# Kernel optimization log

Measured on AMD Instinct MI355X. Metric: run time of the kernel, lower is better.

The kernel has to match this reference:

```python
import jax, jax.numpy as jnp
import numpy as np

# Module hyperparameters (from init_kwargs)
H, E, K = 16, 8, 2          # heads, experts per head, top-k
P, PV = 64, 64              # q/k and v projection sizes
D = 1024                    # state / input / output size
B, T = 8, 512               # batch, sequence length (self-attention)
R = 2 * T - 1               # number of relative offsets


def setup_inputs() -> dict:
    key = jax.random.key(0)
    ks = jax.random.split(key, 9)
    std_in = 1.0 / np.sqrt(D)
    std_out = 1.0 / np.sqrt(H * PV)
    return {
        "x": jax.random.normal(ks[0], (B, T, D), jnp.float32),
        "pe": jax.random.normal(ks[1], (R, D), jnp.float32),
        "w_sel_o": jax.random.normal(ks[2], (H, E, D), jnp.float32) * std_in,
        "w_sel_v": jax.random.normal(ks[3], (H, E, D), jnp.float32) * std_in,
        "W_q": jax.random.normal(ks[4], (H, E, D, P), jnp.float32) * std_in,
        "W_k": jax.random.normal(ks[5], (H, E, D, P), jnp.float32) * std_in,
        "W_v": jax.random.normal(ks[6], (H, E, D, PV), jnp.float32) * std_in,
        "W_o": jax.random.normal(ks[7], (H, E, PV, D), jnp.float32) * std_out,
        "W_pos": jax.random.normal(ks[8], (H * P, D), jnp.float32) * std_in,
    }


def _gates(x, w_sel):
    # sigmoid selection per head, top-K experts kept with their gate values.
    logits = jnp.einsum('btd,hed->bthe', x, w_sel)
    g = jax.nn.sigmoid(logits)
    vals, idx = jax.lax.top_k(g, K)                      # [B,T,H,K]
    onehot = jax.nn.one_hot(idx, E, dtype=g.dtype)        # [B,T,H,K,E]
    return jnp.einsum('bthk,bthke->bthe', vals, onehot)   # sparse dense gates [B,T,H,E]


def _moe_proj(x, W, gates):
    # x [B,T,D], W [H,E,D,P], gates [B,T,H,E] -> [B,T,H,P]
    out = jnp.zeros(x.shape[:2] + (H, W.shape[-1]), x.dtype)
    for e in range(E):  # fixed small expert loop; avoids [B,T,H,E,P] intermediate
        out = out + gates[..., e, None] * jnp.einsum('btd,hdp->bthp', x, W[:, e])
    return out


def reference(x, pe, w_sel_o, w_sel_v, W_q, W_k, W_v, W_o, W_pos):
    # MoEUT selection sharing: q shares o's selection, k shares v's selection.
    g_qo = _gates(x, w_sel_o)
    g_kv = _gates(x, w_sel_v)

    q = _moe_proj(x, W_q, g_qo)   # [B,T,H,P]
    k = _moe_proj(x, W_k, g_kv)   # [B,T,H,P]
    v = _moe_proj(x, W_v, g_kv)   # [B,T,H,PV]

    scale = 1.0 / np.sqrt(P)
    k_pos = (pe @ W_pos.T).reshape(R, H, P)               # relative-position keys

    s_cont = jnp.einsum('bthp,bshp->bhts', q, k)          # content scores
    s_rel = jnp.einsum('bthp,rhp->bhtr', q, k_pos)        # scores over relative offsets
    t_idx = jnp.arange(T)
    rel = t_idx[None, :] - t_idx[:, None] + (T - 1)       # rel index for (t, s)
    s_pos = s_rel[:, :, t_idx[:, None], rel]              # Transformer-XL shift -> [B,H,T,T]

    scores = (s_cont + s_pos) * scale
    causal = t_idx[None, :] <= t_idx[:, None]
    scores = jnp.where(causal[None, None], scores, jnp.asarray(-1e9, scores.dtype))
    attn = jax.nn.softmax(scores, axis=-1)
    ctx = jnp.einsum('bhts,bshv->bthv', attn, v)          # [B,T,H,PV]

    # MoE output projection with o-selection
    out = jnp.zeros((x.shape[0], x.shape[1], W_o.shape[-1]), x.dtype)
    for e in range(E):
        out = out + jnp.einsum('bthv,hvd->btd', ctx * g_qo[..., e, None], W_o[:, e])
    return out
```

## Files before the change

### kernel.cpp

```cpp
#include <hip/hip_runtime.h>
#include <hip/hip_bf16.h>
#include <math.h>

#define H_ 16
#define E_ 8
#define D_ 1024
#define P_ 64
#define PV_ 64
#define B_ 8
#define T_ 512
#define R_ 1023
#define BT_ 4096
#define CAP_ 1024
#define PROWS_ 192
#define PTILES_ 4

typedef __attribute__((ext_vector_type(8))) unsigned short ushort8;
typedef __attribute__((ext_vector_type(4))) unsigned short ushort4v;
typedef __attribute__((ext_vector_type(8))) short short8;
typedef __attribute__((ext_vector_type(4))) float f32x4;

__device__ inline float bf2f(unsigned short u) {
  union { unsigned int i; float f; } c; c.i = ((unsigned int)u) << 16; return c.f;
}
__device__ inline unsigned short f2bf(float f) {
  __hip_bfloat16 h = __float2bfloat16(f);
  return *reinterpret_cast<unsigned short*>(&h);
}

__global__ void zero_cnt_kernel(int* __restrict__ cnt) {
  int i = threadIdx.x;
  if (i < 512) cnt[i] = 0;
}

__global__ __launch_bounds__(256) void xcvt_kernel(
    const float* __restrict__ x, unsigned short* __restrict__ xbu) {
  int i = blockIdx.x * 256 + threadIdx.x;
  float4 w = ((const float4*)x)[i];
  ushort4v o = {f2bf(w.x), f2bf(w.y), f2bf(w.z), f2bf(w.w)};
  *(ushort4v*)&xbu[(size_t)i * 4] = o;
}

__global__ __launch_bounds__(256) void wt_transpose_kernel(
    const float* __restrict__ wso, const float* __restrict__ wsv,
    float* __restrict__ wt) {
  __shared__ float tb[64][65];
  int ct = blockIdx.x, kt = blockIdx.y;
  int tid = threadIdx.x;
  int cl = tid >> 2, kseg = (tid & 3) * 16;
  int c = ct * 64 + cl;
  const float* src = (c < 128) ? (wso + (size_t)c * D_)
                               : (wsv + (size_t)(c - 128) * D_);
#pragma unroll
  for (int i = 0; i < 4; ++i) {
    float4 v4 = *(const float4*)&src[kt * 64 + kseg + i * 4];
    tb[cl][kseg + i * 4 + 0] = v4.x;
    tb[cl][kseg + i * 4 + 1] = v4.y;
    tb[cl][kseg + i * 4 + 2] = v4.z;
    tb[cl][kseg + i * 4 + 3] = v4.w;
  }
  __syncthreads();
  int kl = tid >> 2, cseg = (tid & 3) * 16;
#pragma unroll
  for (int i = 0; i < 4; ++i) {
    float4 o = {tb[cseg + i * 4 + 0][kl], tb[cseg + i * 4 + 1][kl],
                tb[cseg + i * 4 + 2][kl], tb[cseg + i * 4 + 3][kl]};
    *(float4*)&wt[(size_t)(kt * 64 + kl) * 256 + ct * 64 + cseg + i * 4] = o;
  }
}

__global__ __launch_bounds__(256) void gates_gemm(
    const float* __restrict__ x, const float* __restrict__ wt,
    float* __restrict__ part) {
  __shared__ __align__(16) float xs[32][256];
  int tid = threadIdx.x;
  int bt0 = blockIdx.x * 32;
  int ks = blockIdx.y;

  {
    const float4* xr = (const float4*)x;
#pragma unroll
    for (int p = 0; p < 8; ++p) {
      int idx = p * 256 + tid;
      int r = idx >> 6, k4 = idx & 63;
      ((float4*)xs[r])[k4] = xr[(size_t)(bt0 + r) * 256 + ks * 64 + k4];
    }
  }
  __syncthreads();

  int wave = tid >> 6, lane = tid & 63;
  const float4* wt4 = (const float4*)wt + (size_t)ks * 256 * 64 + lane;
  float4 acc[8];
#pragma unroll
  for (int r = 0; r < 8; ++r) acc[r] = (float4){0.f, 0.f, 0.f, 0.f};

  for (int k4b = 0; k4b < 64; ++k4b) {
    float4 wv0 = wt4[(size_t)(k4b * 4 + 0) * 64];
    float4 wv1 = wt4[(size_t)(k4b * 4 + 1) * 64];
    float4 wv2 = wt4[(size_t)(k4b * 4 + 2) * 64];
    float4 wv3 = wt4[(size_t)(k4b * 4 + 3) * 64];
#pragma unroll
    for (int r = 0; r < 8; ++r) {
      float4 xv = ((const float4*)xs[wave * 8 + r])[k4b];
      acc[r].x += xv.x * wv0.x + xv.y * wv1.x + xv.z * wv2.x + xv.w * wv3.x;
      acc[r].y += xv.x * wv0.y + xv.y * wv1.y + xv.z * wv2.y + xv.w * wv3.y;
      acc[r].z += xv.x * wv0.z + xv.y * wv1.z + xv.z * wv2.z + xv.w * wv3.z;
      acc[r].w += xv.x * wv0.w + xv.y * wv1.w + xv.z * wv2.w + xv.w * wv3.w;
    }
  }

#pragma unroll
  for (int r = 0; r < 8; ++r)
    *(float4*)&part[((size_t)(bt0 + wave * 8 + r) * 4 + ks) * 256 + lane * 4] =
        acc[r];
}

__global__ __launch_bounds__(256) void gates_combine(
    const float* __restrict__ part, int* __restrict__ cnt,
    int* __restrict__ lidx, float* __restrict__ lg,
    float* __restrict__ coefs) {
  __shared__ float gv[8][2][H_][E_];
  int tid = threadIdx.x;
  int bt0 = blockIdx.x * 8;

  {
    int set = tid >> 7, he = tid & 127;
    int h = he >> 3, e = he & 7;
#pragma unroll
    for (int r = 0; r < 8; ++r) {
      const float* p = &part[(size_t)(bt0 + r) * 4 * 256 + tid];
      float v = ((p[0] + p[256]) + p[512]) + p[768];
      gv[r][set][h][e] = 1.f / (1.f + expf(-v));
    }
  }
  __syncthreads();

  {
    int r = tid >> 5, st = (tid >> 4) & 1, hh = tid & 15;
    int bt = bt0 + r;
    const float* g = gv[r][st][hh];
    int i1 = 0; float v1 = g[0];
    for (int ee = 1; ee < 8; ee++) if (g[ee] > v1) { v1 = g[ee]; i1 = ee; }
    int i2 = (i1 == 0) ? 1 : 0; float v2 = g[i2];
    for (int ee = 0; ee < 8; ee++) {
      if (ee == i1) continue;
      if (g[ee] > v2) { v2 = g[ee]; i2 = ee; }
    }
    int base1 = ((st * H_ + hh) * E_ + i1) * 2 + 0;
    int p1 = atomicAdd(&cnt[base1], 1);
    lidx[(size_t)base1 * CAP_ + p1] = bt;
    lg[(size_t)base1 * CAP_ + p1] = v1;
    int base2 = ((st * H_ + hh) * E_ + i2) * 2 + 1;
    int p2 = atomicAdd(&cnt[base2], 1);
    lidx[(size_t)base2 * CAP_ + p2] = bt;
    lg[(size_t)base2 * CAP_ + p2] = v2;
    if (st == 0) {
#pragma unroll
      for (int ee = 0; ee < 8; ee++) {
        float c = (ee == i1) ? v1 : ((ee == i2) ? v2 : 0.f);
        coefs[((size_t)bt * H_ + hh) * E_ + ee] = c;
      }
    }
  }
}

__global__ __launch_bounds__(256) void proj_q2_mfma(
    const unsigned short* __restrict__ xb, const float* __restrict__ W,
    const int* __restrict__ cnt, const int* __restrict__ lidx,
    const float* __restrict__ lg, unsigned short* __restrict__ out0,
    unsigned short* __restrict__ out1, int set) {
  int he = blockIdx.x, tile = blockIdx.y;
  int base0 = (set * 128 + he) * 2 + 0, base1 = (set * 128 + he) * 2 + 1;
  int n0 = cnt[base0], n1 = cnt[base1];
  int start = tile * PROWS_;
  if (start >= n0 && start >= n1) return;
  int m0 = min(PROWS_, max(0, n0 - start));
  int m1 = min(PROWS_, max(0, n1 - start));

  __shared__ int ridx0[PROWS_], ridx1[PROWS_];
  __shared__ float rgs0[PROWS_], rgs1[PROWS_];
  __shared__ __align__(16) unsigned short As0[PROWS_][72];
  __shared__ __align__(16) unsigned short As1[PROWS_][72];
  __shared__ __align__(16) unsigned short Bs[64][72];
  int tid = threadIdx.x;
  for (int i = tid; i < PROWS_; i += 256) {
    int v0i = 0, v1i = 0; float g0 = 0.f, g1 = 0.f;
    if (i < m0) {
      v0i = lidx[(size_t)base0 * CAP_ + start + i];
      g0 = lg[(size_t)base0 * CAP_ + start + i];
    }
    if (i < m1) {
      v1i = lidx[(size_t)base1 * CAP_ + start + i];
      g1 = lg[(size_t)base1 * CAP_ + start + i];
    }
    ridx0[i] = v0i; rgs0[i] = g0;
    ridx1[i] = v1i; rgs1[i] = g1;
  }
  __syncthreads();

  int wave = tid >> 6, lane = tid & 63;
  int lr = lane & 15, lk = (lane >> 4) << 3;
  f32x4 acc0[3][4] = {}, acc1[3][4] = {};
  const float* Wb = W + (size_t)he * D_ * P_;

  int sr = tid >> 2, sseg = (tid & 3) << 4;
  int c4 = (tid & 15) * 4;
  int drb = tid >> 4;

  for (int d0 = 0; d0 < D_; d0 += 64) {
#pragma unroll
    for (int i = 0; i < 3; ++i) {
      int row = i * 64 + sr;
      const unsigned short* x0 = xb + (size_t)ridx0[row] * D_ + d0 + sseg;
      *(ushort8*)&As0[row][sseg] = *(const ushort8*)x0;
      *(ushort8*)&As0[row][sseg + 8] = *(const ushort8*)(x0 + 8);
      const unsigned short* x1 = xb + (size_t)ridx1[row] * D_ + d0 + sseg;
      *(ushort8*)&As1[row][sseg] = *(const ushort8*)x1;
      *(ushort8*)&As1[row][sseg + 8] = *(const ushort8*)(x1 + 8);
    }
#pragma unroll
    for (int pass = 0; pass < 4; ++pass) {
      int dr = pass * 16 + drb;
      float4 wv = *(const float4*)&Wb[(size_t)(d0 + dr) * P_ + c4];
      Bs[c4 + 0][dr] = f2bf(wv.x);
      Bs[c4 + 1][dr] = f2bf(wv.y);
      Bs[c4 + 2][dr] = f2bf(wv.z);
      Bs[c4 + 3][dr] = f2bf(wv.w);
    }
    __syncthreads();
#pragma unroll
    for (int kk = 0; kk < 2; ++kk) {
      short8 af0[3], af1[3], bfr[4];
#pragma unroll
      for (int mm = 0; mm < 3; ++mm) {
        af0[mm] = *(const short8*)&As0[wave * 48 + mm * 16 + lr][kk * 32 + lk];
        af1[mm] = *(const short8*)&As1[wave * 48 + mm * 16 + lr][kk * 32 + lk];
      }
#pragma unroll
      for (int nn = 0; nn < 4; ++nn)
        bfr[nn] = *(const short8*)&Bs[nn * 16 + lr][kk * 32 + lk];
#pragma unroll
      for (int mm = 0; mm < 3; ++mm)
#pragma unroll
        for (int nn = 0; nn < 4; ++nn) {
          acc0[mm][nn] = __builtin_amdgcn_mfma_f32_16x16x32_bf16(
              af0[mm], bfr[nn], acc0[mm][nn], 0, 0, 0);
          acc1[mm][nn] = __builtin_amdgcn_mfma_f32_16x16x32_bf16(
              af1[mm], bfr[nn], acc1[mm][nn], 0, 0, 0);
        }
    }
    __syncthreads();
  }

  int h = he >> 3;
#pragma unroll
  for (int mm = 0; mm < 3; ++mm) {
#pragma unroll
    for (int r = 0; r < 4; ++r) {
      int row = wave * 48 + mm * 16 + (lane >> 4) * 4 + r;
      if (row < m0) {
        int bt = ridx0[row]; float g = rgs0[row];
        int b = bt >> 9, t = bt & 511;
        unsigned short* orow = out0 + ((size_t)((b * H_ + h) * T_) + t) * P_;
#pragma unroll
        for (int nn = 0; nn < 4; ++nn)
          orow[nn * 16 + lr] = f2bf(g * acc0[mm][nn][r]);
      }
      if (row < m1) {
        int bt = ridx1[row]; float g = rgs1[row];
        int b = bt >> 9, t = bt & 511;
        unsigned short* orow = out1 + ((size_t)((b * H_ + h) * T_) + t) * P_;
#pragma unroll
        for (int nn = 0; nn < 4; ++nn)
          orow[nn * 16 + lr] = f2bf(g * acc1[mm][nn][r]);
      }
    }
  }
}

__global__ __launch_bounds__(256) void cvt_pos_kernel(
    const float* __restrict__ pe, const float* __restrict__ Wp,
    unsigned short* __restrict__ peb, unsigned short* __restrict__ wpb) {
  int bid = blockIdx.x;
  const float* src;
  unsigned short* dst;
  if (bid < R_) { src = pe + (size_t)bid * D_; dst = peb + (size_t)bid * D_; }
  else { src = Wp + (size_t)(bid - R_) * D_; dst = wpb + (size_t)(bid - R_) * D_; }
  int tid = threadIdx.x;
  float4 w = ((const float4*)src)[tid];
  ushort4v o = {f2bf(w.x), f2bf(w.y), f2bf(w.z), f2bf(w.w)};
  *(ushort4v*)&dst[tid * 4] = o;
}

__global__ __launch_bounds__(256) void kpos_mfma(
    const unsigned short* __restrict__ peb, const unsigned short* __restrict__ wpb,
    unsigned short* __restrict__ kposb) {
  __shared__ __align__(16) unsigned short As[64][72];
  __shared__ __align__(16) unsigned short Bs[64][72];
  int tid = threadIdx.x, mt = blockIdx.x, nt = blockIdx.y;
  int wave = tid >> 6, lane = tid & 63;
  int wr = wave >> 1, wc = wave & 1;
  int lrow = lane & 15, lk = (lane >> 4) << 3;
  f32x4 acc[2][2] = {};
  int sr = tid >> 2, sseg = (tid & 3) << 4;

  for (int d0 = 0; d0 < D_; d0 += 64) {
    {
      const unsigned short* arow = &peb[(size_t)(mt * 64 + sr) * D_ + d0 + sseg];
      *(ushort8*)&As[sr][sseg] = *(const ushort8*)arow;
      *(ushort8*)&As[sr][sseg + 8] = *(const ushort8*)(arow + 8);
      const unsigned short* brow = &wpb[(size_t)(nt * 64 + sr) * D_ + d0 + sseg];
      *(ushort8*)&Bs[sr][sseg] = *(const ushort8*)brow;
      *(ushort8*)&Bs[sr][sseg + 8] = *(const ushort8*)(brow + 8);
    }
    __syncthreads();
#pragma unroll
    for (int kk = 0; kk < 2; ++kk) {
      short8 af[2], bfr[2];
#pragma unroll
      for (int mm = 0; mm < 2; ++mm)
        af[mm] = *(const short8*)&As[wr * 32 + mm * 16 + lrow][kk * 32 + lk];
#pragma unroll
      for (int nn = 0; nn < 2; ++nn)
        bfr[nn] = *(const short8*)&Bs[wc * 32 + nn * 16 + lrow][kk * 32 + lk];
#pragma unroll
      for (int mm = 0; mm < 2; ++mm)
#pragma unroll
        for (int nn = 0; nn < 2; ++nn)
          acc[mm][nn] = __builtin_amdgcn_mfma_f32_16x16x32_bf16(
              af[mm], bfr[nn], acc[mm][nn], 0, 0, 0);
    }
    __syncthreads();
  }

  int orow0 = mt * 64 + wr * 32 + (lane >> 4) * 4;
  int ocol0 = nt * 64 + wc * 32 + lrow;
#pragma unroll
  for (int mm = 0; mm < 2; ++mm)
#pragma unroll
    for (int nn = 0; nn < 2; ++nn)
#pragma unroll
      for (int r = 0; r < 4; ++r)
        kposb[(size_t)(orow0 + mm * 16 + r) * 1024 + ocol0 + nn * 16] =
            f2bf(acc[mm][nn][r]);
}

__global__ __launch_bounds__(256) void attn_mfma(
    const unsigned short* __restrict__ q0, const unsigned short* __restrict__ q1,
    const unsigned short* __restrict__ k0, const unsigned short* __restrict__ k1,
    const unsigned short* __restrict__ v0, const unsigned short* __restrict__ v1,
    const unsigned short* __restrict__ kposb, unsigned short* __restrict__ ctx) {
  int b = blockIdx.x, h = blockIdx.y, qt = blockIdx.z;
  int t0 = qt << 6;
  int tid = threadIdx.x, wave = tid >> 6, lane = tid & 63;
  int lr = lane & 15, lkg = lane >> 4;
  int lk = lkg << 3;

  __shared__ __align__(16) unsigned short Ks[64][72];
  __shared__ __align__(16) unsigned short VTs[64][72];
  __shared__ __align__(16) unsigned short Srl[64][136];

  size_t bh = (size_t)(b * H_ + h);
  const unsigned short* kb0 = k0 + bh * T_ * 64;
  const unsigned short* kb1 = k1 + bh * T_ * 64;
  const unsigned short* vb0 = v0 + bh * T_ * 64;
  const unsigned short* vb1 = v1 + bh * T_ * 64;

  short8 qf[2];
  {
    size_t qoff = (bh * T_ + (size_t)(t0 + wave * 16 + lr)) * 64;
    const unsigned short* q0r = q0 + qoff;
    const unsigned short* q1r = q1 + qoff;
#pragma unroll
    for (int kk = 0; kk < 2; ++kk) {
      ushort8 a0 = *(const ushort8*)&q0r[kk * 32 + lk];
      ushort8 a1 = *(const ushort8*)&q1r[kk * 32 + lk];
      short8 o;
#pragma unroll
      for (int j = 0; j < 8; ++j)
        o[j] = (short)f2bf(bf2f(a0[j]) + bf2f(a1[j]));
      qf[kk] = o;
    }
  }

  float m_run[4], l_run[4];
  f32x4 oacc[4];
#pragma unroll
  for (int r = 0; r < 4; ++r) { m_run[r] = -1e30f; l_run[r] = 0.f; }
#pragma unroll
  for (int nn = 0; nn < 4; ++nn) oacc[nn] = (f32x4){0.f, 0.f, 0.f, 0.f};

  int row_local = wave * 16 + lkg * 4;
  int krow_s = tid >> 1, kseg_s = (tid & 1) * 32;
  int t2 = tid & 127;
  int vr0 = (t2 & 15) * 4, vcs = (t2 >> 4) * 8;

  for (int st = 0; st <= qt; ++st) {
    int s0 = st << 6;
    if (tid < 128) {
      size_t koff = (size_t)(s0 + krow_s) * 64 + kseg_s;
#pragma unroll
      for (int i = 0; i < 4; ++i) {
        ushort8 a0 = *(const ushort8*)(kb0 + koff + i * 8);
        ushort8 a1 = *(const ushort8*)(kb1 + koff + i * 8);
        ushort8 o;
#pragma unroll
        for (int j = 0; j < 8; ++j) o[j] = f2bf(bf2f(a0[j]) + bf2f(a1[j]));
        *(ushort8*)&Ks[krow_s][kseg_s + i * 8] = o;
      }
    } else {
      ushort8 vr[4];
#pragma unroll
      for (int i = 0; i < 4; ++i) {
        size_t voff = (size_t)(s0 + vr0 + i) * 64 + vcs;
        ushort8 a0 = *(const ushort8*)(vb0 + voff);
        ushort8 a1 = *(const ushort8*)(vb1 + voff);
        ushort8 o;
#pragma unroll
        for (int j = 0; j < 8; ++j) o[j] = f2bf(bf2f(a0[j]) + bf2f(a1[j]));
        vr[i] = o;
      }
#pragma unroll
      for (int j = 0; j < 8; ++j) {
        ushort4v o = {vr[0][j], vr[1][j], vr[2][j], vr[3][j]};
        *(ushort4v*)&VTs[vcs + j][vr0] = o;
      }
    }
    __syncthreads();

    f32x4 sc[4] = {};
#pragma unroll
    for (int kk = 0; kk < 2; ++kk) {
#pragma unroll
      for (int nn = 0; nn < 4; ++nn) {
        short8 bfk = *(const short8*)&Ks[nn * 16 + lr][kk * 32 + lk];
        sc[nn] = __builtin_amdgcn_mfma_f32_16x16x32_bf16(qf[kk], bfk, sc[nn], 0, 0, 0);
      }
    }
    int r_base = s0 - t0 + 448;
    const unsigned short* kpb = kposb + (size_t)r_base * 1024 + h * 64;
    f32x4 srf[8] = {};
#pragma unroll
    for (int kk = 0; kk < 2; ++kk) {
#pragma unroll
      for (int nn = 0; nn < 8; ++nn) {
        short8 bfp = *(const short8*)&kpb[(size_t)(nn * 16 + lr) * 1024 + kk * 32 + lk];
        srf[nn] = __builtin_amdgcn_mfma_f32_16x16x32_bf16(qf[kk], bfp, srf[nn], 0, 0, 0);
      }
    }
#pragma unroll
    for (int nn = 0; nn < 8; ++nn)
#pragma unroll
      for (int r = 0; r < 4; ++r)
        Srl[row_local + r][nn * 16 + lr] = f2bf(srf[nn][r]);

    float sv[4][4];
#pragma unroll
    for (int nn = 0; nn < 4; ++nn) {
#pragma unroll
      for (int r = 0; r < 4; ++r) {
        int row = row_local + r;
        int scc = nn * 16 + lr;
        int rj = scc - row + 63;
        float spos = bf2f(Srl[row][rj]);
        float sval = (sc[nn][r] + spos) * 0.125f;
        sv[nn][r] = ((s0 + scc) <= (t0 + row)) ? sval : -1e9f;
      }
    }
    float alpha[4];
#pragma unroll
    for (int r = 0; r < 4; ++r) {
      float mx = fmaxf(fmaxf(sv[0][r], sv[1][r]), fmaxf(sv[2][r], sv[3][r]));
      mx = fmaxf(mx, __shfl_xor(mx, 1));
      mx = fmaxf(mx, __shfl_xor(mx, 2));
      mx = fmaxf(mx, __shfl_xor(mx, 4));
      mx = fmaxf(mx, __shfl_xor(mx, 8));
      float mn = fmaxf(m_run[r], mx);
      alpha[r] = __expf(m_run[r] - mn);
      m_run[r] = mn;
    }
    float psum[4] = {0.f, 0.f, 0.f, 0.f};
#pragma unroll
    for (int nn = 0; nn < 4; ++nn) {
#pragma unroll
      for (int r = 0; r < 4; ++r) {
        unsigned short pb = f2bf(__expf(sv[nn][r] - m_run[r]));
        Srl[row_local + r][64 + nn * 16 + lr] = pb;
        psum[r] += bf2f(pb);
      }
    }
#pragma unroll
    for (int r = 0; r < 4; ++r) {
      float s = psum[r];
      s += __shfl_xor(s, 1); s += __shfl_xor(s, 2);
      s += __shfl_xor(s, 4); s += __shfl_xor(s, 8);
      l_run[r] = l_run[r] * alpha[r] + s;
#pragma unroll
      for (int nn = 0; nn < 4; ++nn) oacc[nn][r] *= alpha[r];
    }
#pragma unroll
    for (int kk = 0; kk < 2; ++kk) {
      short8 pa = *(const short8*)&Srl[wave * 16 + lr][64 + kk * 32 + lk];
#pragma unroll
      for (int nn = 0; nn < 4; ++nn) {
        short8 bv = *(const short8*)&VTs[nn * 16 + lr][kk * 32 + lk];
        oacc[nn] = __builtin_amdgcn_mfma_f32_16x16x32_bf16(pa, bv, oacc[nn], 0, 0, 0);
      }
    }
    __syncthreads();
  }

#pragma unroll
  for (int r = 0; r < 4; ++r) {
    float inv = 1.f / l_run[r];
    int tg = t0 + row_local + r;
    unsigned short* crow = ctx + ((size_t)(b * T_ + tg) * H_ + h) * PV_;
#pragma unroll
    for (int nn = 0; nn < 4; ++nn)
      crow[nn * 16 + lr] = f2bf(oacc[nn][r] * inv);
  }
}

__global__ __launch_bounds__(256) void wo_transpose_kernel(
    const float* __restrict__ Wo, __hip_bfloat16* __restrict__ Wob) {
  __shared__ float t[64][65];
  int kt = blockIdx.x, dt = blockIdx.y;
  int tid = threadIdx.x;
  int kr = tid >> 2, dseg = (tid & 3) * 16;
  const float4* src = (const float4*)&Wo[(size_t)(kt * 64 + kr) * 1024 + dt * 64 + dseg];
#pragma unroll
  for (int i = 0; i < 4; ++i) {
    float4 v4 = src[i];
    t[kr][dseg + i * 4 + 0] = v4.x;
    t[kr][dseg + i * 4 + 1] = v4.y;
    t[kr][dseg + i * 4 + 2] = v4.z;
    t[kr][dseg + i * 4 + 3] = v4.w;
  }
  __syncthreads();
  int dr = tid >> 2, kseg = (tid & 3) * 16;
  unsigned short* dst =
      (unsigned short*)Wob + (size_t)(dt * 64 + dr) * 8192 + kt * 64 + kseg;
#pragma unroll
  for (int half = 0; half < 2; ++half) {
    ushort8 o;
#pragma unroll
    for (int j = 0; j < 8; ++j) o[j] = f2bf(t[kseg + half * 8 + j][dr]);
    *(ushort8*)&dst[half * 8] = o;
  }
}

__global__ __launch_bounds__(256) void moe_out_gemm(
    const __hip_bfloat16* __restrict__ ctx, const float* __restrict__ coefs,
    const __hip_bfloat16* __restrict__ Wob, float* __restrict__ out0,
    float* __restrict__ out1) {
  __shared__ __align__(16) unsigned short As[128][72];
  __shared__ __align__(16) unsigned short Bs[128][72];
  int tid = threadIdx.x;
  int nt = blockIdx.x, mt = blockIdx.y, zh = blockIdx.z;
  int wave = tid >> 6, lane = tid & 63;
  int wr = wave >> 1, wc = wave & 1;
  int lrow = lane & 15, lk = (lane >> 4) << 3;

  f32x4 acc[4][4] = {};

  int arow = tid >> 1, aseg = (tid & 1) * 32;
  const unsigned short* ctxu = (const unsigned short*)ctx;
  const unsigned short* wobu = (const unsigned short*)Wob;
  size_t grow = (size_t)mt * 128 + arow;
  const unsigned short* brp = &wobu[((size_t)nt * 128 + arow) * 8192 + aseg];
  int he0 = zh * 64;

  ushort8 ra[4], rb[4];
  float cf;
  {
    int h = he0 >> 3;
    const ushort8* a = (const ushort8*)&ctxu[(grow * 16 + h) * 64 + aseg];
    const ushort8* bp = (const ushort8*)&brp[(size_t)he0 * 64];
#pragma unroll
    for (int i = 0; i < 4; ++i) { ra[i] = a[i]; rb[i] = bp[i]; }
    cf = coefs[grow * 128 + he0];
  }

  for (int hh = 0; hh < 64; ++hh) {
#pragma unroll
    for (int i = 0; i < 4; ++i) {
      ushort8 o;
#pragma unroll
      for (int j = 0; j < 8; ++j) o[j] = f2bf(bf2f(ra[i][j]) * cf);
      *(ushort8*)&As[arow][aseg + i * 8] = o;
      *(ushort8*)&Bs[arow][aseg + i * 8] = rb[i];
    }
    __syncthreads();

    if (hh < 63) {
      int he = he0 + hh + 1;
      int h = he >> 3;
      const ushort8* a = (const ushort8*)&ctxu[(grow * 16 + h) * 64 + aseg];
      const ushort8* bp = (const ushort8*)&brp[(size_t)he * 64];
#pragma unroll
      for (int i = 0; i < 4; ++i) { ra[i] = a[i]; rb[i] = bp[i]; }
      cf = coefs[grow * 128 + he];
    }

    __builtin_amdgcn_s_setprio(1);
#pragma unroll
    for (int kk = 0; kk < 2; ++kk) {
      short8 af[4], bfr[4];
#pragma unroll
      for (int m = 0; m < 4; ++m)
        af[m] = *(const short8*)&As[wr * 64 + m * 16 + lrow][kk * 32 + lk];
#pragma unroll
      for (int n = 0; n < 4; ++n)
        bfr[n] = *(const short8*)&Bs[wc * 64 + n * 16 + lrow][kk * 32 + lk];
#pragma unroll
      for (int m = 0; m < 4; ++m)
#pragma unroll
        for (int n = 0; n < 4; ++n)
          acc[m][n] = __builtin_amdgcn_mfma_f32_16x16x32_bf16(
              af[m], bfr[n], acc[m][n], 0, 0, 0);
    }
    __builtin_amdgcn_s_setprio(0);
    __syncthreads();
  }

  float* outp = zh ? out1 : out0;
  int orow0 = mt * 128 + wr * 64 + (lane >> 4) * 4;
  int ocol0 = nt * 128 + wc * 64 + lrow;
#pragma unroll
  for (int m = 0; m < 4; ++m)
#pragma unroll
    for (int n = 0; n < 4; ++n)
#pragma unroll
      for (int r = 0; r < 4; ++r)
        outp[(size_t)(orow0 + m * 16 + r) * 1024 + ocol0 + n * 16] = acc[m][n][r];
}

__global__ __launch_bounds__(256) void out_add_kernel(
    float* __restrict__ out, const float* __restrict__ out2) {
  int i = blockIdx.x * 256 + threadIdx.x;
  float4 a = ((const float4*)out)[i];
  float4 b = ((const float4*)out2)[i];
  a.x += b.x; a.y += b.y; a.z += b.z; a.w += b.w;
  ((float4*)out)[i] = a;
}

extern "C" void kernel_launch(void* const* d_in, const int* in_sizes, int n_in,
                              void* d_out, int out_size, void* d_ws, size_t ws_size,
                              hipStream_t stream) {
  const float* x   = (const float*)d_in[0];
  const float* pe  = (const float*)d_in[1];
  const float* wso = (const float*)d_in[2];
  const float* wsv = (const float*)d_in[3];
  const float* Wq  = (const float*)d_in[4];
  const float* Wk  = (const float*)d_in[5];
  const float* Wv  = (const float*)d_in[6];
  const float* Wo  = (const float*)d_in[7];
  const float* Wp  = (const float*)d_in[8];
  float* out = (float*)d_out;
  char* ws = (char*)d_ws;

  int*   cnt   = (int*)  (ws + 0);
  float* coefs = (float*)(ws + 4096);
  int*   lidx  = (int*)  (ws + 2101248);
  float* lg    = (float*)(ws + 4198400);
  unsigned short* xb    = (unsigned short*)(ws + 6295552);
  unsigned short* kposb = (unsigned short*)(ws + 14684160);
  unsigned short* q0    = (unsigned short*)(ws + 16781312);
  unsigned short* q1    = (unsigned short*)(ws + 25169920);
  unsigned short* k0    = (unsigned short*)(ws + 33558528);
  unsigned short* k1    = (unsigned short*)(ws + 41947136);
  unsigned short* v0    = (unsigned short*)(ws + 50335744);
  unsigned short* v1    = (unsigned short*)(ws + 58724352);
  float* part = (float*)(ws + 16781312);
  float* wt   = (float*)(ws + 33558528);
  unsigned short* peb = (unsigned short*)(ws + 41947136);
  unsigned short* wpb = (unsigned short*)(ws + 44044288);
  __hip_bfloat16* ctx = (__hip_bfloat16*)(ws + 6295552);
  __hip_bfloat16* Wob = (__hip_bfloat16*)(ws + 16781312);
  float* out2 = (float*)(ws + 33558528);

  hipLaunchKernelGGL(zero_cnt_kernel, dim3(1), dim3(512), 0, stream, cnt);
  hipLaunchKernelGGL(xcvt_kernel, dim3(4096), dim3(256), 0, stream, x, xb);
  hipLaunchKernelGGL(wt_transpose_kernel, dim3(4, 16), dim3(256), 0, stream,
                     wso, wsv, wt);
  hipLaunchKernelGGL(gates_gemm, dim3(128, 4), dim3(256), 0, stream,
                     x, wt, part);
  hipLaunchKernelGGL(gates_combine, dim3(512), dim3(256), 0, stream,
                     part, cnt, lidx, lg, coefs);

  hipLaunchKernelGGL(cvt_pos_kernel, dim3(R_ + 1024), dim3(256), 0, stream,
                     pe, Wp, peb, wpb);
  hipLaunchKernelGGL(kpos_mfma, dim3(9, 16), dim3(256), 0, stream,
                     peb, wpb, kposb);

  hipLaunchKernelGGL(proj_q2_mfma, dim3(128, PTILES_), dim3(256), 0, stream,
                     xb, Wq, cnt, lidx, lg, q0, q1, 0);
  hipLaunchKernelGGL(proj_q2_mfma, dim3(128, PTILES_), dim3(256), 0, stream,
                     xb, Wk, cnt, lidx, lg, k0, k1, 1);
  hipLaunchKernelGGL(proj_q2_mfma, dim3(128, PTILES_), dim3(256), 0, stream,
                     xb, Wv, cnt, lidx, lg, v0, v1, 1);

  hipLaunchKernelGGL(attn_mfma, dim3(B_, H_, 8), dim3(256), 0, stream,
                     q0, q1, k0, k1, v0, v1, kposb, (unsigned short*)ctx);

  hipLaunchKernelGGL(wo_transpose_kernel, dim3(128, 16), dim3(256), 0, stream,
                     Wo, Wob);
  hipLaunchKernelGGL(moe_out_gemm, dim3(8, 32, 2), dim3(256), 0, stream,
                     ctx, coefs, Wob, out, out2);
  hipLaunchKernelGGL(out_add_kernel, dim3(4096), dim3(256), 0, stream,
                     out, out2);
}
```

Measured before the change: 515.7 us.

## Pre-sum q/k/v partials once and split output GEMM K-range three ways

Adds a separate kernel that sums the two partial q/k/v buffers into one before attention. The attention kernel no longer re-reads and re-adds both halves on every causal K/V tile. The output MoE GEMM is split-K across three z-slices (43/43/42 head-experts) instead of two, giving more blocks for occupancy. The cost is a three-way final reduction that moves more fp32 traffic, plus an extra elementwise pass over q/k/v.

New measurement: 539.4 us. +4.6%, slower.

```diff
diff --git a/kernel.cpp b/kernel.cpp
--- a/kernel.cpp
+++ b/kernel.cpp
@@ -278,6 +278,22 @@
   }
 }
 
+__global__ __launch_bounds__(256) void sum_qkv_kernel(
+    unsigned short* __restrict__ q0, const unsigned short* __restrict__ q1,
+    unsigned short* __restrict__ k0, const unsigned short* __restrict__ k1,
+    unsigned short* __restrict__ v0, const unsigned short* __restrict__ v1) {
+  int arr = blockIdx.y;
+  unsigned short* dst = (arr == 0) ? q0 : (arr == 1) ? k0 : v0;
+  const unsigned short* src = (arr == 0) ? q1 : (arr == 1) ? k1 : v1;
+  size_t i = ((size_t)blockIdx.x * 256 + threadIdx.x) * 8;
+  ushort8 a = *(ushort8*)&dst[i];
+  ushort8 b = *(const ushort8*)&src[i];
+  ushort8 o;
+#pragma unroll
+  for (int j = 0; j < 8; ++j) o[j] = f2bf(bf2f(a[j]) + bf2f(b[j]));
+  *(ushort8*)&dst[i] = o;
+}
+
 __global__ __launch_bounds__(256) void cvt_pos_kernel(
     const float* __restrict__ pe, const float* __restrict__ Wp,
     unsigned short* __restrict__ peb, unsigned short* __restrict__ wpb) {
@@ -346,10 +362,9 @@
 }
 
 __global__ __launch_bounds__(256) void attn_mfma(
-    const unsigned short* __restrict__ q0, const unsigned short* __restrict__ q1,
-    const unsigned short* __restrict__ k0, const unsigned short* __restrict__ k1,
-    const unsigned short* __restrict__ v0, const unsigned short* __restrict__ v1,
-    const unsigned short* __restrict__ kposb, unsigned short* __restrict__ ctx) {
+    const unsigned short* __restrict__ q, const unsigned short* __restrict__ k,
+    const unsigned short* __restrict__ v, const unsigned short* __restrict__ kposb,
+    unsigned short* __restrict__ ctx) {
   int b = blockIdx.x, h = blockIdx.y, qt = blockIdx.z;
   int t0 = qt << 6;
   int tid = threadIdx.x, wave = tid >> 6, lane = tid & 63;
@@ -361,26 +376,15 @@
   __shared__ __align__(16) unsigned short Srl[64][136];
 
   size_t bh = (size_t)(b * H_ + h);
-  const unsigned short* kb0 = k0 + bh * T_ * 64;
-  const unsigned short* kb1 = k1 + bh * T_ * 64;
-  const unsigned short* vb0 = v0 + bh * T_ * 64;
-  const unsigned short* vb1 = v1 + bh * T_ * 64;
+  const unsigned short* kb = k + bh * T_ * 64;
+  const unsigned short* vb = v + bh * T_ * 64;
+  const unsigned short* qb = q + bh * T_ * 64;
 
   short8 qf[2];
   {
-    size_t qoff = (bh * T_ + (size_t)(t0 + wave * 16 + lr)) * 64;
-    const unsigned short* q0r = q0 + qoff;
-    const unsigned short* q1r = q1 + qoff;
-#pragma unroll
-    for (int kk = 0; kk < 2; ++kk) {
-      ushort8 a0 = *(const ushort8*)&q0r[kk * 32 + lk];
-      ushort8 a1 = *(const ushort8*)&q1r[kk * 32 + lk];
-      short8 o;
-#pragma unroll
-      for (int j = 0; j < 8; ++j)
-        o[j] = (short)f2bf(bf2f(a0[j]) + bf2f(a1[j]));
-      qf[kk] = o;
-    }
+    const unsigned short* qrow = qb + (size_t)(t0 + wave * 16 + lr) * 64;
+    qf[0] = *(const short8*)&qrow[lk];
+    qf[1] = *(const short8*)&qrow[32 + lk];
   }
 
   float m_run[4], l_run[4];
@@ -398,28 +402,15 @@
   for (int st = 0; st <= qt; ++st) {
     int s0 = st << 6;
     if (tid < 128) {
-      size_t koff = (size_t)(s0 + krow_s) * 64 + kseg_s;
-#pragma unroll
-      for (int i = 0; i < 4; ++i) {
-        ushort8 a0 = *(const ushort8*)(kb0 + koff + i * 8);
-        ushort8 a1 = *(const ushort8*)(kb1 + koff + i * 8);
-        ushort8 o;
-#pragma unroll
-        for (int j = 0; j < 8; ++j) o[j] = f2bf(bf2f(a0[j]) + bf2f(a1[j]));
-        *(ushort8*)&Ks[krow_s][kseg_s + i * 8] = o;
-      }
+      const unsigned short* krow = kb + (size_t)(s0 + krow_s) * 64 + kseg_s;
+#pragma unroll
+      for (int i = 0; i < 4; ++i)
+        *(ushort8*)&Ks[krow_s][kseg_s + i * 8] = *(const ushort8*)(krow + i * 8);
     } else {
       ushort8 vr[4];
 #pragma unroll
-      for (int i = 0; i < 4; ++i) {
-        size_t voff = (size_t)(s0 + vr0 + i) * 64 + vcs;
-        ushort8 a0 = *(const ushort8*)(vb0 + voff);
-        ushort8 a1 = *(const ushort8*)(vb1 + voff);
-        ushort8 o;
-#pragma unroll
-        for (int j = 0; j < 8; ++j) o[j] = f2bf(bf2f(a0[j]) + bf2f(a1[j]));
-        vr[i] = o;
-      }
+      for (int i = 0; i < 4; ++i)
+        vr[i] = *(const ushort8*)&vb[(size_t)(s0 + vr0 + i) * 64 + vcs];
 #pragma unroll
       for (int j = 0; j < 8; ++j) {
         ushort4v o = {vr[0][j], vr[1][j], vr[2][j], vr[3][j]};
@@ -552,7 +543,7 @@
 __global__ __launch_bounds__(256) void moe_out_gemm(
     const __hip_bfloat16* __restrict__ ctx, const float* __restrict__ coefs,
     const __hip_bfloat16* __restrict__ Wob, float* __restrict__ out0,
-    float* __restrict__ out1) {
+    float* __restrict__ out1, float* __restrict__ out2) {
   __shared__ __align__(16) unsigned short As[128][72];
   __shared__ __align__(16) unsigned short Bs[128][72];
   int tid = threadIdx.x;
@@ -568,7 +559,8 @@
   const unsigned short* wobu = (const unsigned short*)Wob;
   size_t grow = (size_t)mt * 128 + arow;
   const unsigned short* brp = &wobu[((size_t)nt * 128 + arow) * 8192 + aseg];
-  int he0 = zh * 64;
+  int he0 = (zh == 0) ? 0 : (zh == 1) ? 43 : 86;
+  int hcnt = (zh == 2) ? 42 : 43;
 
   ushort8 ra[4], rb[4];
   float cf;
@@ -581,7 +573,7 @@
     cf = coefs[grow * 128 + he0];
   }
 
-  for (int hh = 0; hh < 64; ++hh) {
+  for (int hh = 0; hh < hcnt; ++hh) {
 #pragma unroll
     for (int i = 0; i < 4; ++i) {
       ushort8 o;
@@ -592,7 +584,7 @@
     }
     __syncthreads();
 
-    if (hh < 63) {
+    if (hh < hcnt - 1) {
       int he = he0 + hh + 1;
       int h = he >> 3;
       const ushort8* a = (const ushort8*)&ctxu[(grow * 16 + h) * 64 + aseg];
@@ -623,7 +615,7 @@
     __syncthreads();
   }
 
-  float* outp = zh ? out1 : out0;
+  float* outp = (zh == 0) ? out0 : (zh == 1) ? out1 : out2;
   int orow0 = mt * 128 + wr * 64 + (lane >> 4) * 4;
   int ocol0 = nt * 128 + wc * 64 + lrow;
 #pragma unroll
@@ -635,12 +627,17 @@
         outp[(size_t)(orow0 + m * 16 + r) * 1024 + ocol0 + n * 16] = acc[m][n][r];
 }
 
-__global__ __launch_bounds__(256) void out_add_kernel(
-    float* __restrict__ out, const float* __restrict__ out2) {
+__global__ __launch_bounds__(256) void out_add3_kernel(
+    float* __restrict__ out, const float* __restrict__ out2,
+    const float* __restrict__ out3) {
   int i = blockIdx.x * 256 + threadIdx.x;
   float4 a = ((const float4*)out)[i];
   float4 b = ((const float4*)out2)[i];
-  a.x += b.x; a.y += b.y; a.z += b.z; a.w += b.w;
+  float4 c = ((const float4*)out3)[i];
+  a.x = (a.x + b.x) + c.x;
+  a.y = (a.y + b.y) + c.y;
+  a.z = (a.z + b.z) + c.z;
+  a.w = (a.w + b.w) + c.w;
   ((float4*)out)[i] = a;
 }
 
@@ -678,6 +675,7 @@
   __hip_bfloat16* ctx = (__hip_bfloat16*)(ws + 6295552);
   __hip_bfloat16* Wob = (__hip_bfloat16*)(ws + 16781312);
   float* out2 = (float*)(ws + 33558528);
+  float* out3 = (float*)(ws + 50335744);
 
   hipLaunchKernelGGL(zero_cnt_kernel, dim3(1), dim3(512), 0, stream, cnt);
   hipLaunchKernelGGL(xcvt_kernel, dim3(4096), dim3(256), 0, stream, x, xb);
@@ -700,13 +698,16 @@
   hipLaunchKernelGGL(proj_q2_mfma, dim3(128, PTILES_), dim3(256), 0, stream,
                      xb, Wv, cnt, lidx, lg, v0, v1, 1);
 
+  hipLaunchKernelGGL(sum_qkv_kernel, dim3(2048, 3), dim3(256), 0, stream,
+                     q0, q1, k0, k1, v0, v1);
+
   hipLaunchKernelGGL(attn_mfma, dim3(B_, H_, 8), dim3(256), 0, stream,
-                     q0, q1, k0, k1, v0, v1, kposb, (unsigned short*)ctx);
+                     q0, k0, v0, kposb, (unsigned short*)ctx);
 
   hipLaunchKernelGGL(wo_transpose_kernel, dim3(128, 16), dim3(256), 0, stream,
                      Wo, Wob);
-  hipLaunchKernelGGL(moe_out_gemm, dim3(8, 32, 2), dim3(256), 0, stream,
-                     ctx, coefs, Wob, out, out2);
-  hipLaunchKernelGGL(out_add_kernel, dim3(4096), dim3(256), 0, stream,
-                     out, out2);
-}
+  hipLaunchKernelGGL(moe_out_gemm, dim3(8, 32, 3), dim3(256), 0, stream,
+                     ctx, coefs, Wob, out, out2, out3);
+  hipLaunchKernelGGL(out_add3_kernel, dim3(4096), dim3(256), 0, stream,
+                     out, out2, out3);
+}
```
